# Kernel tuning notes

Measured on AMD Instinct MI355X. Metric: run time of the kernel, lower is better.

The kernel has to match this reference:

```python
import jax, jax.numpy as jnp
import numpy as np

N, E = 50000, 800000
IN_DIM = 256
OUT_DIM = 256
H = 8
D = OUT_DIM // H  # head_dim = 32
SCALE = D ** -0.5
LN_EPS = 1e-5


def _layernorm(x, g, b):
    mu = jnp.mean(x, axis=-1, keepdims=True)
    var = jnp.mean((x - mu) ** 2, axis=-1, keepdims=True)
    return (x - mu) * jax.lax.rsqrt(var + LN_EPS) * g + b


def setup_inputs() -> dict:
    key = jax.random.key(0)
    ks = jax.random.split(key, 12)
    s = 1.0 / np.sqrt(IN_DIM)
    inp = {
        "x": jax.random.normal(ks[0], (N, IN_DIM), jnp.float32),
        "edge_index": jax.random.randint(ks[1], (2, E), 0, N, jnp.int64),
        "batch": jnp.zeros((N,), jnp.int64),
        # weights stored (in, out) so forward is x @ W
        "Wq": jax.random.uniform(ks[2], (IN_DIM, OUT_DIM), jnp.float32, -s, s),
        "Wk": jax.random.uniform(ks[3], (IN_DIM, OUT_DIM), jnp.float32, -s, s),
        "Wv": jax.random.uniform(ks[4], (IN_DIM, OUT_DIM), jnp.float32, -s, s),
        "Wo_w": jax.random.uniform(ks[5], (OUT_DIM, OUT_DIM), jnp.float32, -s, s),
        "Wo_b": jnp.zeros((OUT_DIM,), jnp.float32),
        "ln1_g": jnp.ones((OUT_DIM,), jnp.float32),
        "ln1_b": jnp.zeros((OUT_DIM,), jnp.float32),
        "ln2_g": jnp.ones((OUT_DIM,), jnp.float32),
        "ln2_b": jnp.zeros((OUT_DIM,), jnp.float32),
        "ffn_w1": jax.random.uniform(ks[6], (OUT_DIM, 2 * OUT_DIM), jnp.float32, -s, s),
        "ffn_b1": jnp.zeros((2 * OUT_DIM,), jnp.float32),
        "ffn_w2": jax.random.uniform(ks[7], (2 * OUT_DIM, OUT_DIM), jnp.float32, -s, s),
        "ffn_b2": jnp.zeros((OUT_DIM,), jnp.float32),
    }
    return inp


def reference(x, edge_index, batch, Wq, Wk, Wv, Wo_w, Wo_b, ln1_g, ln1_b,
              ln2_g, ln2_b, ffn_w1, ffn_b1, ffn_w2, ffn_b2):
    n = x.shape[0]
    residual = x  # in_dim == out_dim -> Identity residual_proj
    Q = (x @ Wq).reshape(n, H, D)
    K = (x @ Wk).reshape(n, H, D)
    V = (x @ Wv).reshape(n, H, D)
    src, dst = edge_index[0], edge_index[1]

    # edge scores (E, H)
    scores = jnp.einsum('ehd,ehd->eh', Q[dst], K[src]) * SCALE
    # segmented max per destination node; init zeros matches torch
    # scatter_reduce amax with include_self=True on a zeros buffer
    attn_max = jnp.zeros((n, H), scores.dtype).at[dst].max(scores)
    w = jnp.exp(scores - attn_max[dst])
    attn_sum = jnp.zeros((n, H), w.dtype).at[dst].add(w)
    w = w / (attn_sum[dst] + 1e-8)

    msg = V[src] * w[:, :, None]                      # (E, H, D)
    out = jnp.zeros((n, H, D), msg.dtype).at[dst].add(msg)
    out = out.reshape(n, OUT_DIM) @ Wo_w + Wo_b

    out = _layernorm(residual + out, ln1_g, ln1_b)
    ffn = jax.nn.gelu(out @ ffn_w1 + ffn_b1, approximate=False) @ ffn_w2 + ffn_b2
    out = _layernorm(out + ffn, ln2_g, ln2_b)
    return out
```

## Files before the change

kernel.cpp:

```cpp
#include <hip/hip_runtime.h>
#include <hip/hip_bf16.h>
#include <math.h>

#define NNODES 50000
#define NEDGES 800000
#define DIM 256
#define HID_DIM 512

typedef short bf16x8 __attribute__((ext_vector_type(8)));
typedef float f32x4 __attribute__((ext_vector_type(4)));

__device__ __forceinline__ float bf2f(unsigned short u) {
    return __uint_as_float(((unsigned)u) << 16);
}
__device__ __forceinline__ unsigned short f2bf_u16(float v) {
    __hip_bfloat16 h = __float2bfloat16(v);
    return __builtin_bit_cast(unsigned short, h);
}
__device__ __forceinline__ void unpack8(uint4 v, float* f) {
    f[0] = __uint_as_float(v.x << 16); f[1] = __uint_as_float(v.x & 0xffff0000u);
    f[2] = __uint_as_float(v.y << 16); f[3] = __uint_as_float(v.y & 0xffff0000u);
    f[4] = __uint_as_float(v.z << 16); f[5] = __uint_as_float(v.z & 0xffff0000u);
    f[6] = __uint_as_float(v.w << 16); f[7] = __uint_as_float(v.w & 0xffff0000u);
}
__device__ __forceinline__ unsigned pk2(float a, float b) {
    return (unsigned)f2bf_u16(a) | ((unsigned)f2bf_u16(b) << 16);
}
__device__ __forceinline__ uint4 pack8(const float* f) {
    return make_uint4(pk2(f[0],f[1]), pk2(f[2],f[3]), pk2(f[4],f[5]), pk2(f[6],f[7]));
}

#define GLD(g, l) __builtin_amdgcn_global_load_lds( \
    (const __attribute__((address_space(1))) unsigned int*)(g), \
    (__attribute__((address_space(3))) unsigned int*)(l), 16, 0, 0)

template <int MODE>
__global__ __launch_bounds__(256) void gemm_bf16_kernel(
    const __hip_bfloat16* __restrict__ A,
    const __hip_bfloat16* __restrict__ BT,
    const float* __restrict__ bias,
    const void* __restrict__ resid,
    const float* __restrict__ gam, const float* __restrict__ bet,
    __hip_bfloat16* __restrict__ Ch,
    float* __restrict__ Cf,
    int M, int K, int Nc)
{
    __shared__ __align__(16) char ldsbuf[40960];
    short* As = (short*)ldsbuf;
    short* Bs = (short*)(ldsbuf + 8192);
    short* Cs = (short*)ldsbuf;
    float* red = (float*)(ldsbuf + 33792);

    const int nTilesN = Nc >> 8;
    const int bm = blockIdx.x / nTilesN;
    const int bn = blockIdx.x - bm * nTilesN;
    const int m0 = bm << 6, n0 = bn << 8;
    const int t = threadIdx.x;
    const int wave = t >> 6, lane = t & 63;
    const int quad = lane >> 4, l16 = lane & 15;
    const int wn = wave << 6;

    f32x4 acc[4][4] = {};

    const int rr = lane >> 3, chk = lane & 7;
    const int gcol = (chk ^ rr) << 3;
    size_t aoff[2], boff[8];
    #pragma unroll
    for (int g = 0; g < 2; ++g) {
        int gm = m0 + (wave * 2 + g) * 8 + rr;
        if (gm >= M) gm = M - 1;
        aoff[g] = (size_t)gm * K + gcol;
    }
    #pragma unroll
    for (int g = 0; g < 8; ++g)
        boff[g] = (size_t)(n0 + (wave * 8 + g) * 8 + rr) * K + gcol;

    for (int k0 = 0; k0 < K; k0 += 64) {
        #pragma unroll
        for (int g = 0; g < 2; ++g)
            GLD(A + aoff[g] + k0, &As[(wave * 2 + g) * 512]);
        #pragma unroll
        for (int g = 0; g < 8; ++g)
            GLD(BT + boff[g] + k0, &Bs[(wave * 8 + g) * 512]);
        __syncthreads();
        #pragma unroll
        for (int kk = 0; kk < 2; ++kk) {
            const int cswz = quad + kk * 4;
            bf16x8 af[4], bfv[4];
            #pragma unroll
            for (int i = 0; i < 4; ++i) {
                int row = i * 16 + l16;
                af[i] = *(const bf16x8*)(&As[row * 64 + ((cswz ^ (row & 7)) << 3)]);
            }
            #pragma unroll
            for (int j = 0; j < 4; ++j) {
                int row = wn + j * 16 + l16;
                bfv[j] = *(const bf16x8*)(&Bs[row * 64 + ((cswz ^ (row & 7)) << 3)]);
            }
            #pragma unroll
            for (int i = 0; i < 4; ++i)
                #pragma unroll
                for (int j = 0; j < 4; ++j)
                    acc[i][j] = __builtin_amdgcn_mfma_f32_16x16x32_bf16(af[i], bfv[j], acc[i][j], 0, 0, 0);
        }
        __syncthreads();
    }

    float bv[4];
    #pragma unroll
    for (int j = 0; j < 4; ++j)
        bv[j] = bias ? bias[n0 + wn + j * 16 + l16] : 0.f;

    if constexpr (MODE <= 1) {
        #pragma unroll
        for (int i = 0; i < 4; ++i)
            #pragma unroll
            for (int j = 0; j < 4; ++j) {
                int col = wn + j * 16 + l16;
                #pragma unroll
                for (int r = 0; r < 4; ++r) {
                    int row = i * 16 + quad * 4 + r;
                    float v = acc[i][j][r] + bv[j];
                    if (MODE == 1) v = 0.5f * v * (1.f + erff(v * 0.70710678118654752f));
                    Cs[row * 264 + col] = (short)f2bf_u16(v);
                }
            }
        __syncthreads();
        #pragma unroll
        for (int it = 0; it < 8; ++it) {
            int ci = it * 256 + t;
            int row = ci >> 5, ck = ci & 31;
            int gm = m0 + row;
            if (gm < M) {
                uint4 v = *(const uint4*)(&Cs[row * 264 + ck * 8]);
                *(uint4*)(&Ch[(size_t)gm * Nc + n0 + ck * 8]) = v;
            }
        }
    } else {
        #pragma unroll
        for (int i = 0; i < 4; ++i)
            #pragma unroll
            for (int r = 0; r < 4; ++r) {
                int rowg = m0 + i * 16 + quad * 4 + r;
                int rc = rowg < M ? rowg : M - 1;
                #pragma unroll
                for (int j = 0; j < 4; ++j) {
                    int col = wn + j * 16 + l16;
                    float rv;
                    if constexpr (MODE == 2)
                        rv = ((const float*)resid)[(size_t)rc * 256 + col];
                    else
                        rv = bf2f(((const unsigned short*)resid)[(size_t)rc * 256 + col]);
                    acc[i][j][r] += bv[j] + rv;
                }
            }
        #pragma unroll
        for (int i = 0; i < 4; ++i)
            #pragma unroll
            for (int r = 0; r < 4; ++r) {
                float ss = (acc[i][0][r] + acc[i][1][r]) + (acc[i][2][r] + acc[i][3][r]);
                float qq = (acc[i][0][r]*acc[i][0][r] + acc[i][1][r]*acc[i][1][r])
                         + (acc[i][2][r]*acc[i][2][r] + acc[i][3][r]*acc[i][3][r]);
                ss += __shfl_xor(ss, 1); ss += __shfl_xor(ss, 2);
                ss += __shfl_xor(ss, 4); ss += __shfl_xor(ss, 8);
                qq += __shfl_xor(qq, 1); qq += __shfl_xor(qq, 2);
                qq += __shfl_xor(qq, 4); qq += __shfl_xor(qq, 8);
                if (l16 == 0) {
                    int row = i * 16 + quad * 4 + r;
                    red[row * 4 + wave]       = ss;
                    red[256 + row * 4 + wave] = qq;
                }
            }
        __syncthreads();
        float mean_[4][4], inv_[4][4];
        #pragma unroll
        for (int i = 0; i < 4; ++i)
            #pragma unroll
            for (int r = 0; r < 4; ++r) {
                int row = i * 16 + quad * 4 + r;
                float4 sv = *(const float4*)&red[row * 4];
                float4 qv = *(const float4*)&red[256 + row * 4];
                float s  = (sv.x + sv.y) + (sv.z + sv.w);
                float q  = (qv.x + qv.y) + (qv.z + qv.w);
                float mean = s * (1.f / 256.f);
                float var  = q * (1.f / 256.f) - mean * mean;
                mean_[i][r] = mean;
                inv_[i][r]  = rsqrtf(var + 1e-5f);
            }
        float gv[4], btv[4];
        #pragma unroll
        for (int j = 0; j < 4; ++j) {
            int col = wn + j * 16 + l16;
            gv[j] = gam[col]; btv[j] = bet[col];
        }
        if constexpr (MODE == 2) {
            #pragma unroll
            for (int i = 0; i < 4; ++i)
                #pragma unroll
                for (int j = 0; j < 4; ++j) {
                    int col = wn + j * 16 + l16;
                    #pragma unroll
                    for (int r = 0; r < 4; ++r) {
                        int row = i * 16 + quad * 4 + r;
                        float v = (acc[i][j][r] - mean_[i][r]) * inv_[i][r] * gv[j] + btv[j];
                        Cs[row * 264 + col] = (short)f2bf_u16(v);
                    }
                }
            __syncthreads();
            #pragma unroll
            for (int it = 0; it < 8; ++it) {
                int ci = it * 256 + t;
                int row = ci >> 5, ck = ci & 31;
                int gm = m0 + row;
                if (gm < M) {
                    uint4 v = *(const uint4*)(&Cs[row * 264 + ck * 8]);
                    *(uint4*)(&Ch[(size_t)gm * 256 + ck * 8]) = v;
                }
            }
        } else {
            #pragma unroll
            for (int i = 0; i < 4; ++i)
                #pragma unroll
                for (int r = 0; r < 4; ++r) {
                    int rowg = m0 + i * 16 + quad * 4 + r;
                    if (rowg < M) {
                        #pragma unroll
                        for (int j = 0; j < 4; ++j) {
                            int col = wn + j * 16 + l16;
                            float v = (acc[i][j][r] - mean_[i][r]) * inv_[i][r] * gv[j] + btv[j];
                            Cf[(size_t)rowg * 256 + col] = v;
                        }
                    }
                }
        }
    }
}

__global__ void conv_bf16_kernel(const float* __restrict__ in,
                                 __hip_bfloat16* __restrict__ out, int n4)
{
    int i = blockIdx.x * 256 + threadIdx.x;
    if (i < n4) {
        float4 v = ((const float4*)in)[i];
        float f[4] = {v.x, v.y, v.z, v.w};
        uint2 o = make_uint2(pk2(f[0], f[1]), pk2(f[2], f[3]));
        ((uint2*)out)[i] = o;
    }
}

__global__ __launch_bounds__(256) void prep_w_kernel(
    const float* __restrict__ Wq, const float* __restrict__ Wk,
    const float* __restrict__ Wv, const float* __restrict__ Wo,
    const float* __restrict__ f1, const float* __restrict__ f2,
    unsigned short* __restrict__ WqkvT, unsigned short* __restrict__ WoT,
    unsigned short* __restrict__ f1T, unsigned short* __restrict__ f2T)
{
    __shared__ unsigned short Ts[64 * 72];
    int b = blockIdx.x, t = threadIdx.x;
    const float* S; unsigned short* D; int K, N, tile;
    if (b < 64) {
        int m = b >> 4; tile = b & 15; K = 256; N = 256;
        S = (m == 0) ? Wq : (m == 1) ? Wk : (m == 2) ? Wv : Wo;
        D = (m == 3) ? WoT : WqkvT + m * 65536;
    } else if (b < 96) { tile = b - 64; S = f1; D = f1T; K = 256; N = 512; }
    else               { tile = b - 96; S = f2; D = f2T; K = 512; N = 256; }
    int tilesN = N >> 6;
    int k0 = (tile / tilesN) << 6, n0 = (tile % tilesN) << 6;
    #pragma unroll
    for (int it = 0; it < 16; ++it) {
        int idx = it * 256 + t;
        int r = idx >> 6, c = idx & 63;
        Ts[r * 72 + c] = f2bf_u16(S[(size_t)(k0 + r) * N + n0 + c]);
    }
    __syncthreads();
    #pragma unroll
    for (int it = 0; it < 16; ++it) {
        int idx = it * 256 + t;
        int r = idx >> 6, c = idx & 63;
        D[(size_t)(n0 + r) * K + k0 + c] = Ts[c * 72 + r];
    }
}

__global__ void hist_kernel(const int* __restrict__ dst, int* __restrict__ counts, int E)
{
    int e = blockIdx.x * blockDim.x + threadIdx.x;
    if (e < E) atomicAdd(&counts[dst[e]], 1);
}

__global__ void scan1_kernel(const int* __restrict__ counts, int* __restrict__ starts,
                             int* __restrict__ bsums, int N)
{
    __shared__ int tmp[256];
    int t = threadIdx.x;
    int i = blockIdx.x * 256 + t;
    int v = (i < N) ? counts[i] : 0;
    tmp[t] = v;
    __syncthreads();
    for (int off = 1; off < 256; off <<= 1) {
        int add = (t >= off) ? tmp[t - off] : 0;
        __syncthreads();
        tmp[t] += add;
        __syncthreads();
    }
    if (i < N) starts[i] = tmp[t] - v;
    if (t == 255) bsums[blockIdx.x] = tmp[255];
}

__global__ void scan2_kernel(const int* __restrict__ bsums, int* __restrict__ bexc, int NB)
{
    __shared__ int tmp[256];
    int t = threadIdx.x;
    int v = (t < NB) ? bsums[t] : 0;
    tmp[t] = v;
    __syncthreads();
    for (int off = 1; off < 256; off <<= 1) {
        int add = (t >= off) ? tmp[t - off] : 0;
        __syncthreads();
        tmp[t] += add;
        __syncthreads();
    }
    bexc[t] = tmp[t] - v;
}

__global__ void scan3_kernel(int* __restrict__ starts, const int* __restrict__ bexc,
                             const int* __restrict__ counts, int* __restrict__ cursor, int N)
{
    int t = threadIdx.x;
    int i = blockIdx.x * 256 + t;
    if (i < N) {
        int val = starts[i] + bexc[blockIdx.x];
        starts[i] = val;
        cursor[i] = val;
        if (i == N - 1) starts[N] = val + counts[i];
    }
}

__global__ void scatter_kernel(const int* __restrict__ src, const int* __restrict__ dst,
                               int* __restrict__ cursor, int* __restrict__ csr_src, int E)
{
    int e = blockIdx.x * blockDim.x + threadIdx.x;
    if (e < E) {
        int d = dst[e];
        int slot = atomicAdd(&cursor[d], 1);
        csr_src[slot] = src[e];
    }
}

__global__ __launch_bounds__(256) void attn_kernel(
    const __hip_bfloat16* __restrict__ QKV,
    const int* __restrict__ starts, const int* __restrict__ csr_src,
    __hip_bfloat16* __restrict__ out)
{
    const int n = blockIdx.x * 4 + (threadIdx.x >> 6);
    const int lane = threadIdx.x & 63;
    const int half = lane >> 5;
    const int c = (lane & 31) << 3;
    const size_t qb = (size_t)n * 768;
    uint4 qv = *(const uint4*)(QKV + qb + c);
    float q[8]; unpack8(qv, q);
    const int beg = starts[n], end = starts[n + 1];
    const float SC = 0.17677669529663688f;

    float l0 = 0.f, l1 = 0.f;
    float a0[8] = {0,0,0,0,0,0,0,0};
    float a1[8] = {0,0,0,0,0,0,0,0};
    for (int e = beg; e < end; e += 4) {
        int e0 = e + half, e1 = e + 2 + half;
        int s0 = csr_src[min(e0, end - 1)];
        int s1 = csr_src[min(e1, end - 1)];
        float m0 = (e0 < end) ? 1.f : 0.f;
        float m1 = (e1 < end) ? 1.f : 0.f;
        const __hip_bfloat16* p0 = QKV + (size_t)s0 * 768 + 256 + c;
        const __hip_bfloat16* p1 = QKV + (size_t)s1 * 768 + 256 + c;
        uint4 k0 = *(const uint4*)p0;
        uint4 k1 = *(const uint4*)p1;
        uint4 v0 = *(const uint4*)(p0 + 256);
        uint4 v1 = *(const uint4*)(p1 + 256);
        float kk[8], vv[8];
        unpack8(k0, kk);
        float d0 = q[0]*kk[0] + q[1]*kk[1] + q[2]*kk[2] + q[3]*kk[3]
                 + q[4]*kk[4] + q[5]*kk[5] + q[6]*kk[6] + q[7]*kk[7];
        unpack8(k1, kk);
        float d1 = q[0]*kk[0] + q[1]*kk[1] + q[2]*kk[2] + q[3]*kk[3]
                 + q[4]*kk[4] + q[5]*kk[5] + q[6]*kk[6] + q[7]*kk[7];
        d0 += __shfl_xor(d0, 1); d0 += __shfl_xor(d0, 2);
        d1 += __shfl_xor(d1, 1); d1 += __shfl_xor(d1, 2);
        float p0s = __expf(d0 * SC) * m0;
        float p1s = __expf(d1 * SC) * m1;
        l0 += p0s; l1 += p1s;
        unpack8(v0, vv);
        #pragma unroll
        for (int k = 0; k < 8; ++k) a0[k] += p0s * vv[k];
        unpack8(v1, vv);
        #pragma unroll
        for (int k = 0; k < 8; ++k) a1[k] += p1s * vv[k];
    }
    float l = l0 + l1;
    l += __shfl_xor(l, 32);
    float o[8];
    #pragma unroll
    for (int k = 0; k < 8; ++k) {
        float v = a0[k] + a1[k];
        v += __shfl_xor(v, 32);
        o[k] = v;
    }
    float inv = 1.f / (l + 1e-8f);
    #pragma unroll
    for (int k = 0; k < 8; ++k) o[k] *= inv;
    if (half == 0)
        *(uint4*)(out + (size_t)n * DIM + c) = pack8(o);
}

extern "C" void kernel_launch(void* const* d_in, const int* in_sizes, int n_in,
                              void* d_out, int out_size, void* d_ws, size_t ws_size,
                              hipStream_t stream)
{
    const float* x     = (const float*)d_in[0];
    const int*   edge  = (const int*)d_in[1];
    const float* Wq    = (const float*)d_in[3];
    const float* Wk    = (const float*)d_in[4];
    const float* Wv    = (const float*)d_in[5];
    const float* Wo_w  = (const float*)d_in[6];
    const float* Wo_b  = (const float*)d_in[7];
    const float* ln1_g = (const float*)d_in[8];
    const float* ln1_b = (const float*)d_in[9];
    const float* ln2_g = (const float*)d_in[10];
    const float* ln2_b = (const float*)d_in[11];
    const float* fw1   = (const float*)d_in[12];
    const float* fb1   = (const float*)d_in[13];
    const float* fw2   = (const float*)d_in[14];
    const float* fb2   = (const float*)d_in[15];
    const int* srcA = edge;
    const int* dstA = edge + NEDGES;

    char* p = (char*)d_ws;
    __hip_bfloat16* QKVh = (__hip_bfloat16*)p;  p += (size_t)NNODES * 768 * 2;
    __hip_bfloat16* AOh  = (__hip_bfloat16*)p;  p += (size_t)NNODES * DIM * 2;
    __hip_bfloat16* O1h  = (__hip_bfloat16*)p;  p += (size_t)NNODES * DIM * 2;
    __hip_bfloat16* HIDh = (__hip_bfloat16*)p;  p += (size_t)NNODES * HID_DIM * 2;
    __hip_bfloat16* xh   = (__hip_bfloat16*)p;  p += (size_t)NNODES * DIM * 2;
    unsigned short* WqkvT = (unsigned short*)p; p += (size_t)768 * 256 * 2;
    unsigned short* WoT   = (unsigned short*)p; p += (size_t)256 * 256 * 2;
    unsigned short* f1T   = (unsigned short*)p; p += (size_t)512 * 256 * 2;
    unsigned short* f2T   = (unsigned short*)p; p += (size_t)256 * 512 * 2;
    int* counts = (int*)p;  p += sizeof(int) * NNODES;
    int* starts = (int*)p;  p += sizeof(int) * (NNODES + 1);
    int* bsums  = (int*)p;  p += sizeof(int) * 256;
    int* bexc   = (int*)p;  p += sizeof(int) * 256;
    int* cursor = (int*)p;  p += sizeof(int) * NNODES;
    int* csr    = (int*)p;  p += sizeof(int) * NEDGES;

    const int NB = (NNODES + 255) / 256;
    const int mT = (NNODES + 63) / 64;
    dim3 blk(256);

    conv_bf16_kernel<<<(NNODES * DIM / 4 + 255) / 256, blk, 0, stream>>>(x, xh, NNODES * DIM / 4);
    prep_w_kernel<<<128, blk, 0, stream>>>(Wq, Wk, Wv, Wo_w, fw1, fw2, WqkvT, WoT, f1T, f2T);

    hipMemsetAsync(counts, 0, sizeof(int) * NNODES, stream);
    hist_kernel<<<(NEDGES + 255) / 256, blk, 0, stream>>>(dstA, counts, NEDGES);
    scan1_kernel<<<NB, blk, 0, stream>>>(counts, starts, bsums, NNODES);
    scan2_kernel<<<1, blk, 0, stream>>>(bsums, bexc, NB);
    scan3_kernel<<<NB, blk, 0, stream>>>(starts, bexc, counts, cursor, NNODES);
    scatter_kernel<<<(NEDGES + 255) / 256, blk, 0, stream>>>(srcA, dstA, cursor, csr, NEDGES);

    gemm_bf16_kernel<0><<<mT * 3, blk, 0, stream>>>(
        xh, (const __hip_bfloat16*)WqkvT, nullptr, nullptr, nullptr, nullptr,
        QKVh, nullptr, NNODES, 256, 768);

    attn_kernel<<<NNODES / 4, blk, 0, stream>>>(QKVh, starts, csr, AOh);

    gemm_bf16_kernel<2><<<mT, blk, 0, stream>>>(
        AOh, (const __hip_bfloat16*)WoT, Wo_b, x, ln1_g, ln1_b,
        O1h, nullptr, NNODES, 256, 256);

    gemm_bf16_kernel<1><<<mT * 2, blk, 0, stream>>>(
        O1h, (const __hip_bfloat16*)f1T, fb1, nullptr, nullptr, nullptr,
        HIDh, nullptr, NNODES, 256, 512);

    gemm_bf16_kernel<3><<<mT, blk, 0, stream>>>(
        HIDh, (const __hip_bfloat16*)f2T, fb2, O1h, ln2_g, ln2_b,
        nullptr, (float*)d_out, NNODES, 512, 256);
}
```

Baseline: 515.2 us.

## Load GEMM fragments directly from global memory, dropping LDS staging

```diff
diff --git a/kernel.cpp b/kernel.cpp
--- a/kernel.cpp
+++ b/kernel.cpp
@@ -29,10 +29,6 @@
 __device__ __forceinline__ uint4 pack8(const float* f) {
     return make_uint4(pk2(f[0],f[1]), pk2(f[2],f[3]), pk2(f[4],f[5]), pk2(f[6],f[7]));
 }
-
-#define GLD(g, l) __builtin_amdgcn_global_load_lds( \
-    (const __attribute__((address_space(1))) unsigned int*)(g), \
-    (__attribute__((address_space(3))) unsigned int*)(l), 16, 0, 0)
 
 template <int MODE>
 __global__ __launch_bounds__(256) void gemm_bf16_kernel(
@@ -45,9 +41,7 @@
     float* __restrict__ Cf,
     int M, int K, int Nc)
 {
-    __shared__ __align__(16) char ldsbuf[40960];
-    short* As = (short*)ldsbuf;
-    short* Bs = (short*)(ldsbuf + 8192);
+    __shared__ __align__(16) char ldsbuf[35840];
     short* Cs = (short*)ldsbuf;
     float* red = (float*)(ldsbuf + 33792);
 
@@ -62,48 +56,31 @@
 
     f32x4 acc[4][4] = {};
 
-    const int rr = lane >> 3, chk = lane & 7;
-    const int gcol = (chk ^ rr) << 3;
-    size_t aoff[2], boff[8];
-    #pragma unroll
-    for (int g = 0; g < 2; ++g) {
-        int gm = m0 + (wave * 2 + g) * 8 + rr;
-        if (gm >= M) gm = M - 1;
-        aoff[g] = (size_t)gm * K + gcol;
-    }
-    #pragma unroll
-    for (int g = 0; g < 8; ++g)
-        boff[g] = (size_t)(n0 + (wave * 8 + g) * 8 + rr) * K + gcol;
-
-    for (int k0 = 0; k0 < K; k0 += 64) {
-        #pragma unroll
-        for (int g = 0; g < 2; ++g)
-            GLD(A + aoff[g] + k0, &As[(wave * 2 + g) * 512]);
-        #pragma unroll
-        for (int g = 0; g < 8; ++g)
-            GLD(BT + boff[g] + k0, &Bs[(wave * 8 + g) * 512]);
-        __syncthreads();
-        #pragma unroll
-        for (int kk = 0; kk < 2; ++kk) {
-            const int cswz = quad + kk * 4;
-            bf16x8 af[4], bfv[4];
-            #pragma unroll
-            for (int i = 0; i < 4; ++i) {
-                int row = i * 16 + l16;
-                af[i] = *(const bf16x8*)(&As[row * 64 + ((cswz ^ (row & 7)) << 3)]);
-            }
-            #pragma unroll
-            for (int j = 0; j < 4; ++j) {
-                int row = wn + j * 16 + l16;
-                bfv[j] = *(const bf16x8*)(&Bs[row * 64 + ((cswz ^ (row & 7)) << 3)]);
-            }
-            #pragma unroll
-            for (int i = 0; i < 4; ++i)
-                #pragma unroll
-                for (int j = 0; j < 4; ++j)
-                    acc[i][j] = __builtin_amdgcn_mfma_f32_16x16x32_bf16(af[i], bfv[j], acc[i][j], 0, 0, 0);
-        }
-        __syncthreads();
+    unsigned aoff[4], boff[4];
+    #pragma unroll
+    for (int i = 0; i < 4; ++i) {
+        int rm = m0 + i * 16 + l16;
+        if (rm >= M) rm = M - 1;
+        aoff[i] = (unsigned)rm * K + quad * 8;
+    }
+    #pragma unroll
+    for (int j = 0; j < 4; ++j)
+        boff[j] = (unsigned)(n0 + wn + j * 16 + l16) * K + quad * 8;
+
+    #pragma unroll 2
+    for (int k0 = 0; k0 < K; k0 += 32) {
+        bf16x8 af[4], bfv[4];
+        #pragma unroll
+        for (int i = 0; i < 4; ++i)
+            af[i] = *(const bf16x8*)(A + aoff[i] + k0);
+        #pragma unroll
+        for (int j = 0; j < 4; ++j)
+            bfv[j] = *(const bf16x8*)(BT + boff[j] + k0);
+        #pragma unroll
+        for (int i = 0; i < 4; ++i)
+            #pragma unroll
+            for (int j = 0; j < 4; ++j)
+                acc[i][j] = __builtin_amdgcn_mfma_f32_16x16x32_bf16(af[i], bfv[j], acc[i][j], 0, 0, 0);
     }
 
     float bv[4];
```

New measurement: 599.6 us. 1.16x slower.

## Add persistent GEMM keeping weight slice in LDS for QKV and FFN1

Applied to the files above, without the earlier changes.

```diff
diff --git a/kernel.cpp b/kernel.cpp
--- a/kernel.cpp
+++ b/kernel.cpp
@@ -33,6 +33,95 @@
 #define GLD(g, l) __builtin_amdgcn_global_load_lds( \
     (const __attribute__((address_space(1))) unsigned int*)(g), \
     (__attribute__((address_space(3))) unsigned int*)(l), 16, 0, 0)
+
+template <int MODE>
+__global__ __launch_bounds__(256) void gemm_persist_kernel(
+    const __hip_bfloat16* __restrict__ A,
+    const __hip_bfloat16* __restrict__ BT,
+    const float* __restrict__ bias,
+    __hip_bfloat16* __restrict__ Ch,
+    int M, int Nc, int nsl, int mstride)
+{
+    constexpr int K = 256;
+    constexpr int CH = K / 8;
+    __shared__ short Bs[128 * K];
+
+    const int slice = blockIdx.x % nsl;
+    const int chunk = blockIdx.x / nsl;
+    const int n0 = slice << 7;
+    const int t = threadIdx.x;
+    const int lane = t & 63;
+    const int quad = lane >> 4, l16 = lane & 15;
+    const int wn2 = (t >> 6) << 5;
+
+    #pragma unroll
+    for (int it = 0; it < 16; ++it) {
+        int idx = it * 256 + t;
+        int row = idx >> 5, c = idx & (CH - 1);
+        uint4 v = *(const uint4*)(BT + (size_t)(n0 + row) * K + c * 8);
+        *(uint4*)(&Bs[row * K + ((c ^ (row & 7)) << 3)]) = v;
+    }
+    __syncthreads();
+
+    float bvv[2][4];
+    #pragma unroll
+    for (int j = 0; j < 2; ++j)
+        #pragma unroll
+        for (int r = 0; r < 4; ++r)
+            bvv[j][r] = bias ? bias[n0 + wn2 + j * 16 + quad * 4 + r] : 0.f;
+
+    const int NTM = (M + 63) >> 6;
+    for (int mt = chunk; mt < NTM; mt += mstride) {
+        const int m0 = mt << 6;
+        const __hip_bfloat16* abase[4];
+        #pragma unroll
+        for (int i = 0; i < 4; ++i) {
+            int rm = m0 + i * 16 + l16;
+            if (rm >= M) rm = M - 1;
+            abase[i] = A + (size_t)rm * K + quad * 8;
+        }
+        f32x4 acc[4][2] = {};
+        #pragma unroll
+        for (int ks = 0; ks < 8; ++ks) {
+            bf16x8 af[4], bfv[2];
+            #pragma unroll
+            for (int i = 0; i < 4; ++i)
+                af[i] = *(const bf16x8*)(abase[i] + ks * 32);
+            #pragma unroll
+            for (int j = 0; j < 2; ++j) {
+                int row = wn2 + j * 16 + l16;
+                int kc = ks * 4 + quad;
+                bfv[j] = *(const bf16x8*)(&Bs[row * K + ((kc ^ (row & 7)) << 3)]);
+            }
+            #pragma unroll
+            for (int i = 0; i < 4; ++i)
+                #pragma unroll
+                for (int j = 0; j < 2; ++j)
+                    acc[i][j] = __builtin_amdgcn_mfma_f32_16x16x32_bf16(bfv[j], af[i], acc[i][j], 0, 0, 0);
+        }
+        #pragma unroll
+        for (int i = 0; i < 4; ++i) {
+            int m = m0 + i * 16 + l16;
+            if (m < M) {
+                #pragma unroll
+                for (int j = 0; j < 2; ++j) {
+                    float v0 = acc[i][j][0] + bvv[j][0];
+                    float v1 = acc[i][j][1] + bvv[j][1];
+                    float v2 = acc[i][j][2] + bvv[j][2];
+                    float v3 = acc[i][j][3] + bvv[j][3];
+                    if (MODE == 1) {
+                        v0 = 0.5f * v0 * (1.f + erff(v0 * 0.70710678118654752f));
+                        v1 = 0.5f * v1 * (1.f + erff(v1 * 0.70710678118654752f));
+                        v2 = 0.5f * v2 * (1.f + erff(v2 * 0.70710678118654752f));
+                        v3 = 0.5f * v3 * (1.f + erff(v3 * 0.70710678118654752f));
+                    }
+                    uint2 o = make_uint2(pk2(v0, v1), pk2(v2, v3));
+                    *(uint2*)(&Ch[(size_t)m * Nc + n0 + wn2 + j * 16 + quad * 4]) = o;
+                }
+            }
+        }
+    }
+}
 
 template <int MODE>
 __global__ __launch_bounds__(256) void gemm_bf16_kernel(
@@ -111,7 +200,63 @@
     for (int j = 0; j < 4; ++j)
         bv[j] = bias ? bias[n0 + wn + j * 16 + l16] : 0.f;
 
-    if constexpr (MODE <= 1) {
+    #pragma unroll
+    for (int i = 0; i < 4; ++i)
+        #pragma unroll
+        for (int r = 0; r < 4; ++r) {
+            int rowg = m0 + i * 16 + quad * 4 + r;
+            int rc = rowg < M ? rowg : M - 1;
+            #pragma unroll
+            for (int j = 0; j < 4; ++j) {
+                int col = wn + j * 16 + l16;
+                float rv;
+                if constexpr (MODE == 2)
+                    rv = ((const float*)resid)[(size_t)rc * 256 + col];
+                else
+                    rv = bf2f(((const unsigned short*)resid)[(size_t)rc * 256 + col]);
+                acc[i][j][r] += bv[j] + rv;
+            }
+        }
+    #pragma unroll
+    for (int i = 0; i < 4; ++i)
+        #pragma unroll
+        for (int r = 0; r < 4; ++r) {
+            float ss = (acc[i][0][r] + acc[i][1][r]) + (acc[i][2][r] + acc[i][3][r]);
+            float qq = (acc[i][0][r]*acc[i][0][r] + acc[i][1][r]*acc[i][1][r])
+                     + (acc[i][2][r]*acc[i][2][r] + acc[i][3][r]*acc[i][3][r]);
+            ss += __shfl_xor(ss, 1); ss += __shfl_xor(ss, 2);
+            ss += __shfl_xor(ss, 4); ss += __shfl_xor(ss, 8);
+            qq += __shfl_xor(qq, 1); qq += __shfl_xor(qq, 2);
+            qq += __shfl_xor(qq, 4); qq += __shfl_xor(qq, 8);
+            if (l16 == 0) {
+                int row = i * 16 + quad * 4 + r;
+                red[row * 4 + wave]       = ss;
+                red[256 + row * 4 + wave] = qq;
+            }
+        }
+    __syncthreads();
+    float mean_[4][4], inv_[4][4];
+    #pragma unroll
+    for (int i = 0; i < 4; ++i)
+        #pragma unroll
+        for (int r = 0; r < 4; ++r) {
+            int row = i * 16 + quad * 4 + r;
+            float4 sv = *(const float4*)&red[row * 4];
+            float4 qv = *(const float4*)&red[256 + row * 4];
+            float s  = (sv.x + sv.y) + (sv.z + sv.w);
+            float q  = (qv.x + qv.y) + (qv.z + qv.w);
+            float mean = s * (1.f / 256.f);
+            float var  = q * (1.f / 256.f) - mean * mean;
+            mean_[i][r] = mean;
+            inv_[i][r]  = rsqrtf(var + 1e-5f);
+        }
+    float gv[4], btv[4];
+    #pragma unroll
+    for (int j = 0; j < 4; ++j) {
+        int col = wn + j * 16 + l16;
+        gv[j] = gam[col]; btv[j] = bet[col];
+    }
+    if constexpr (MODE == 2) {
         #pragma unroll
         for (int i = 0; i < 4; ++i)
             #pragma unroll
@@ -120,8 +265,7 @@
                 #pragma unroll
                 for (int r = 0; r < 4; ++r) {
                     int row = i * 16 + quad * 4 + r;
-                    float v = acc[i][j][r] + bv[j];
-                    if (MODE == 1) v = 0.5f * v * (1.f + erff(v * 0.70710678118654752f));
+                    float v = (acc[i][j][r] - mean_[i][r]) * inv_[i][r] * gv[j] + btv[j];
                     Cs[row * 264 + col] = (short)f2bf_u16(v);
                 }
             }
@@ -133,7 +277,7 @@
             int gm = m0 + row;
             if (gm < M) {
                 uint4 v = *(const uint4*)(&Cs[row * 264 + ck * 8]);
-                *(uint4*)(&Ch[(size_t)gm * Nc + n0 + ck * 8]) = v;
+                *(uint4*)(&Ch[(size_t)gm * 256 + ck * 8]) = v;
             }
         }
     } else {
@@ -142,97 +286,15 @@
             #pragma unroll
             for (int r = 0; r < 4; ++r) {
                 int rowg = m0 + i * 16 + quad * 4 + r;
-                int rc = rowg < M ? rowg : M - 1;
-                #pragma unroll
-                for (int j = 0; j < 4; ++j) {
-                    int col = wn + j * 16 + l16;
-                    float rv;
-                    if constexpr (MODE == 2)
-                        rv = ((const float*)resid)[(size_t)rc * 256 + col];
-                    else
-                        rv = bf2f(((const unsigned short*)resid)[(size_t)rc * 256 + col]);
-                    acc[i][j][r] += bv[j] + rv;
-                }
-            }
-        #pragma unroll
-        for (int i = 0; i < 4; ++i)
-            #pragma unroll
-            for (int r = 0; r < 4; ++r) {
-                float ss = (acc[i][0][r] + acc[i][1][r]) + (acc[i][2][r] + acc[i][3][r]);
-                float qq = (acc[i][0][r]*acc[i][0][r] + acc[i][1][r]*acc[i][1][r])
-                         + (acc[i][2][r]*acc[i][2][r] + acc[i][3][r]*acc[i][3][r]);
-                ss += __shfl_xor(ss, 1); ss += __shfl_xor(ss, 2);
-                ss += __shfl_xor(ss, 4); ss += __shfl_xor(ss, 8);
-                qq += __shfl_xor(qq, 1); qq += __shfl_xor(qq, 2);
-                qq += __shfl_xor(qq, 4); qq += __shfl_xor(qq, 8);
-                if (l16 == 0) {
-                    int row = i * 16 + quad * 4 + r;
-                    red[row * 4 + wave]       = ss;
-                    red[256 + row * 4 + wave] = qq;
-                }
-            }
-        __syncthreads();
-        float mean_[4][4], inv_[4][4];
-        #pragma unroll
-        for (int i = 0; i < 4; ++i)
-            #pragma unroll
-            for (int r = 0; r < 4; ++r) {
-                int row = i * 16 + quad * 4 + r;
-                float4 sv = *(const float4*)&red[row * 4];
-                float4 qv = *(const float4*)&red[256 + row * 4];
-                float s  = (sv.x + sv.y) + (sv.z + sv.w);
-                float q  = (qv.x + qv.y) + (qv.z + qv.w);
-                float mean = s * (1.f / 256.f);
-                float var  = q * (1.f / 256.f) - mean * mean;
-                mean_[i][r] = mean;
-                inv_[i][r]  = rsqrtf(var + 1e-5f);
-            }
-        float gv[4], btv[4];
-        #pragma unroll
-        for (int j = 0; j < 4; ++j) {
-            int col = wn + j * 16 + l16;
-            gv[j] = gam[col]; btv[j] = bet[col];
-        }
-        if constexpr (MODE == 2) {
-            #pragma unroll
-            for (int i = 0; i < 4; ++i)
-                #pragma unroll
-                for (int j = 0; j < 4; ++j) {
-                    int col = wn + j * 16 + l16;
+                if (rowg < M) {
                     #pragma unroll
-                    for (int r = 0; r < 4; ++r) {
-                        int row = i * 16 + quad * 4 + r;
+                    for (int j = 0; j < 4; ++j) {
+                        int col = wn + j * 16 + l16;
                         float v = (acc[i][j][r] - mean_[i][r]) * inv_[i][r] * gv[j] + btv[j];
-                        Cs[row * 264 + col] = (short)f2bf_u16(v);
+                        Cf[(size_t)rowg * 256 + col] = v;
                     }
                 }
-            __syncthreads();
-            #pragma unroll
-            for (int it = 0; it < 8; ++it) {
-                int ci = it * 256 + t;
-                int row = ci >> 5, ck = ci & 31;
-                int gm = m0 + row;
-                if (gm < M) {
-                    uint4 v = *(const uint4*)(&Cs[row * 264 + ck * 8]);
-                    *(uint4*)(&Ch[(size_t)gm * 256 + ck * 8]) = v;
-                }
-            }
-        } else {
-            #pragma unroll
-            for (int i = 0; i < 4; ++i)
-                #pragma unroll
-                for (int r = 0; r < 4; ++r) {
-                    int rowg = m0 + i * 16 + quad * 4 + r;
-                    if (rowg < M) {
-                        #pragma unroll
-                        for (int j = 0; j < 4; ++j) {
-                            int col = wn + j * 16 + l16;
-                            float v = (acc[i][j][r] - mean_[i][r]) * inv_[i][r] * gv[j] + btv[j];
-                            Cf[(size_t)rowg * 256 + col] = v;
-                        }
-                    }
-                }
-        }
+            }
     }
 }
 
@@ -464,9 +526,8 @@
     scan3_kernel<<<NB, blk, 0, stream>>>(starts, bexc, counts, cursor, NNODES);
     scatter_kernel<<<(NEDGES + 255) / 256, blk, 0, stream>>>(srcA, dstA, cursor, csr, NEDGES);
 
-    gemm_bf16_kernel<0><<<mT * 3, blk, 0, stream>>>(
-        xh, (const __hip_bfloat16*)WqkvT, nullptr, nullptr, nullptr, nullptr,
-        QKVh, nullptr, NNODES, 256, 768);
+    gemm_persist_kernel<0><<<6 * 85, blk, 0, stream>>>(
+        xh, (const __hip_bfloat16*)WqkvT, nullptr, QKVh, NNODES, 768, 6, 85);
 
     attn_kernel<<<NNODES / 4, blk, 0, stream>>>(QKVh, starts, csr, AOh);
 
@@ -474,9 +535,8 @@
         AOh, (const __hip_bfloat16*)WoT, Wo_b, x, ln1_g, ln1_b,
         O1h, nullptr, NNODES, 256, 256);
 
-    gemm_bf16_kernel<1><<<mT * 2, blk, 0, stream>>>(
-        O1h, (const __hip_bfloat16*)f1T, fb1, nullptr, nullptr, nullptr,
-        HIDh, nullptr, NNODES, 256, 512);
+    gemm_persist_kernel<1><<<4 * 128, blk, 0, stream>>>(
+        O1h, (const __hip_bfloat16*)f1T, fb1, HIDh, NNODES, 512, 4, 128);
 
     gemm_bf16_kernel<3><<<mT, blk, 0, stream>>>(
         HIDh, (const __hip_bfloat16*)f2T, fb2, O1h, ln2_g, ln2_b,
```

New measurement: 578.3 us. 1.12x slower.
